# Kernel optimization log

Hardware: AMD Instinct MI355X
Metric: run time of the kernel (lower is better)

The kernel has to match this reference:

```python
import jax, jax.numpy as jnp
import numpy as np

B, V, C, H, W, D = 2, 3, 8, 128, 160, 64


def bilinear_sample(feat, grid):
    """feat: [B,C,H,W]; grid: [B,N,2] normalized to [-1,1], align_corners=True,
    padding_mode='zeros' (matches F.grid_sample). Returns [B,C,N]."""
    b, c, h, w = feat.shape
    ix = (grid[..., 0] + 1.0) * 0.5 * (w - 1)  # [B,N]
    iy = (grid[..., 1] + 1.0) * 0.5 * (h - 1)
    x0 = jnp.floor(ix)
    y0 = jnp.floor(iy)
    wx1 = ix - x0
    wy1 = iy - y0
    flat = feat.reshape(b, c, h * w)

    def corner(xi, yi, wgt):
        valid = (xi >= 0) & (xi <= w - 1) & (yi >= 0) & (yi <= h - 1)
        xc = jnp.clip(xi, 0, w - 1).astype(jnp.int32)
        yc = jnp.clip(yi, 0, h - 1).astype(jnp.int32)
        idx = yc * w + xc  # [B,N]
        vals = jnp.take_along_axis(flat, jnp.broadcast_to(idx[:, None, :], (b, c, idx.shape[1])), axis=2)
        return vals * (wgt * valid.astype(feat.dtype))[:, None, :]

    out = (corner(x0, y0, (1 - wx1) * (1 - wy1))
           + corner(x0 + 1, y0, wx1 * (1 - wy1))
           + corner(x0, y0 + 1, (1 - wx1) * wy1)
           + corner(x0 + 1, y0 + 1, wx1 * wy1))
    return out


def homo_warping(src_feat, proj_mat, depth_values):
    """src_feat [B,C,H,W], proj_mat [B,3,4], depth_values [B,D,H,W].
    Returns warped volume [B,C,D,H,W] and normalized grid [B,D,H,W,2]."""
    b, c, h, w = src_feat.shape
    d = depth_values.shape[1]
    R = proj_mat[:, :, :3]
    T = proj_mat[:, :, 3:]  # [B,3,1]
    ys, xs = jnp.meshgrid(jnp.arange(h, dtype=src_feat.dtype),
                          jnp.arange(w, dtype=src_feat.dtype), indexing='ij')
    ref = jnp.stack([xs.ravel(), ys.ravel(), jnp.ones(h * w, src_feat.dtype)], 0)  # [3,HW]
    Rp = jnp.einsum('bij,jp->bip', R, ref)  # [B,3,HW]
    dv = depth_values.reshape(b, d, h * w)
    src = Rp[:, :, None, :] + T[:, :, :, None] / dv[:, None, :, :]  # [B,3,D,HW]
    xy = src[:, :2] / src[:, 2:3]
    gx = xy[:, 0] / ((w - 1) / 2.0) - 1.0
    gy = xy[:, 1] / ((h - 1) / 2.0) - 1.0
    grid = jnp.stack([gx, gy], axis=-1)  # [B,D,HW,2]
    warped = bilinear_sample(src_feat, grid.reshape(b, d * h * w, 2)).reshape(b, c, d, h, w)
    return warped, grid.reshape(b, d, h, w, 2)


def setup_inputs() -> dict:
    key = jax.random.key(0)
    k1, k2, k3, k4, k5 = jax.random.split(key, 5)
    features = jax.random.normal(k1, (V, B, C, H, W), dtype=jnp.float32)
    # near-identity projective maps so warps land mostly in-bounds
    eye = jnp.broadcast_to(jnp.eye(3, dtype=jnp.float32), (B, V, 3, 3))
    Rm = eye + 0.01 * jax.random.normal(k2, (B, V, 3, 3), dtype=jnp.float32)
    Tm = 2.0 * jax.random.normal(k3, (B, V, 3, 1), dtype=jnp.float32)
    proj_matrices = jnp.concatenate([Rm, Tm], axis=-1)  # [B,V,3,4]
    base = jnp.linspace(2.0, 10.0, D, dtype=jnp.float32)[None, :, None, None]
    depth_values = base + 0.1 * jax.random.uniform(k4, (B, D, H, W), dtype=jnp.float32)
    reg_weight = jax.random.normal(k5, (C,), dtype=jnp.float32)
    return {"features": features, "proj_matrices": proj_matrices,
            "depth_values": depth_values, "reg_weight": reg_weight,
            "num_depth": D}


def reference(features, proj_matrices, depth_values, reg_weight, num_depth):
    v = features.shape[0]
    ref_feat = features[0]
    b, c, h, w = ref_feat.shape
    d = num_depth
    ref_volume = jnp.broadcast_to(ref_feat[:, :, None], (b, c, d, h, w))
    volume_sum = ref_volume
    volume_sq_sum = ref_volume ** 2
    in_masks = jnp.ones((b, 1, d, h, w), dtype=ref_feat.dtype)
    for i in range(1, v):  # fixed small number of source views
        warped, grid = homo_warping(features[i], proj_matrices[:, i], depth_values)
        m = (grid > -1.0) & (grid < 1.0)
        in_masks = in_masks + (m[..., 0] & m[..., 1]).astype(ref_feat.dtype)[:, None]
        volume_sum = volume_sum + warped
        volume_sq_sum = volume_sq_sum + warped ** 2
    count = 1.0 / in_masks
    volume_feat = volume_sq_sum * count - (volume_sum * count) ** 2  # [B,C,D,H,W]
    # stand-in cost regularization: channel reduction -> [B,D,H,W]
    cost = jnp.einsum('bcdhw,c->bdhw', volume_feat, reg_weight)
    prob_volume = jax.nn.softmax(cost, axis=1)
    depth = jnp.sum(prob_volume * depth_values, axis=1)  # [B,H,W]
    return depth
```

## Files before the change

kernel.cpp:

```cpp
#include <hip/hip_runtime.h>
#include <math.h>

#define BB 2
#define VV 3
#define CC 8
#define HH 128
#define WW 160
#define DD 64
constexpr int HW = HH * WW;
constexpr int NPIX = BB * HW;
constexpr int PIXBANDS = NPIX / 256;
constexpr int BANDS_PER_XCD = PIXBANDS / 8;

typedef _Float16 h8 __attribute__((ext_vector_type(8)));

static __device__ __forceinline__ h8 splat8(float x) {
    const _Float16 v = (_Float16)x;
    h8 r = {v, v, v, v, v, v, v, v};
    return r;
}

__global__ __launch_bounds__(256)
void transpose_feats(const float* __restrict__ feats, h8* __restrict__ ft)
{
    const int t = blockIdx.x * blockDim.x + threadIdx.x;
    if (t >= VV * BB * HW) return;
    const int vb = t / HW;
    const int hw = t - vb * HW;
    const float* src = feats + (size_t)vb * CC * HW + hw;
    h8 v;
#pragma unroll
    for (int c = 0; c < CC; ++c) v[c] = (_Float16)src[(size_t)c * HW];
    ft[(size_t)vb * HW + hw] = v;
}

__global__ __launch_bounds__(256)
void cost_kernel(const h8* __restrict__ ft,
                 const float* __restrict__ proj,
                 const float* __restrict__ depthv,
                 const float* __restrict__ regw,
                 float* __restrict__ cost_out)
{
    const int i    = blockIdx.x;
    const int xcd  = i & 7;
    const int idx  = i >> 3;
    const int band = xcd * BANDS_PER_XCD + (idx % BANDS_PER_XCD);
    const int d    = idx / BANDS_PER_XCD;
    const int pixel = band * 256 + threadIdx.x;

    const int b  = (pixel >= HW) ? 1 : 0;
    const int hw = pixel - b * HW;
    const int h  = hw / WW;
    const int w  = hw - h * WW;

    float rf[CC], rf2[CC];
    {
        h8 rv = ft[(size_t)b * HW + hw];
#pragma unroll
        for (int c = 0; c < CC; ++c) { rf[c] = (float)rv[c]; rf2[c] = rf[c] * rf[c]; }
    }

    float Rp[2][3], Tv[2][3];
    const float xf = (float)w, yf = (float)h;
#pragma unroll
    for (int v = 0; v < 2; ++v) {
        const float* M = proj + ((size_t)b * VV + (v + 1)) * 12;
#pragma unroll
        for (int j = 0; j < 3; ++j) {
            Rp[v][j] = M[j * 4 + 0] * xf + M[j * 4 + 1] * yf + M[j * 4 + 2];
            Tv[v][j] = M[j * 4 + 3];
        }
    }

    const h8* fsrc0 = ft + (size_t)(1 * BB + b) * HW;
    const h8* fsrc1 = ft + (size_t)(2 * BB + b) * HW;

    const float dv = depthv[(size_t)b * DD * HW + (size_t)d * HW + hw];
    const float inv_dv = __builtin_amdgcn_rcpf(dv);

    float wt[2][4];
    int   ib[2][4];
    float nmask = 1.0f;
#pragma unroll
    for (int v = 0; v < 2; ++v) {
        const float sx = Rp[v][0] + Tv[v][0] * inv_dv;
        const float sy = Rp[v][1] + Tv[v][1] * inv_dv;
        const float sz = Rp[v][2] + Tv[v][2] * inv_dv;
        const float rsz = __builtin_amdgcn_rcpf(sz);
        const float ix = sx * rsz;
        const float iy = sy * rsz;
        nmask += ((ix > 0.f) && (ix < (float)(WW - 1)) &&
                  (iy > 0.f) && (iy < (float)(HH - 1))) ? 1.0f : 0.0f;
        const float x0f = floorf(ix), y0f = floorf(iy);
        const float wx1 = ix - x0f, wy1 = iy - y0f;
        const float wx0 = 1.f - wx1, wy0 = 1.f - wy1;
        const float x1f = x0f + 1.f, y1f = y0f + 1.f;
        const bool vx0 = (x0f >= 0.f) && (x0f <= (float)(WW - 1));
        const bool vx1 = (x1f >= 0.f) && (x1f <= (float)(WW - 1));
        const bool vy0 = (y0f >= 0.f) && (y0f <= (float)(HH - 1));
        const bool vy1 = (y1f >= 0.f) && (y1f <= (float)(HH - 1));
        wt[v][0] = wx0 * wy0 * ((vx0 && vy0) ? 1.f : 0.f);
        wt[v][1] = wx1 * wy0 * ((vx1 && vy0) ? 1.f : 0.f);
        wt[v][2] = wx0 * wy1 * ((vx0 && vy1) ? 1.f : 0.f);
        wt[v][3] = wx1 * wy1 * ((vx1 && vy1) ? 1.f : 0.f);
        const int x0c = (int)fminf(fmaxf(x0f, 0.f), (float)(WW - 1));
        const int x1c = (int)fminf(fmaxf(x1f, 0.f), (float)(WW - 1));
        const int y0c = (int)fminf(fmaxf(y0f, 0.f), (float)(HH - 1));
        const int y1c = (int)fminf(fmaxf(y1f, 0.f), (float)(HH - 1));
        ib[v][0] = y0c * WW + x0c;
        ib[v][1] = y0c * WW + x1c;
        ib[v][2] = y1c * WW + x0c;
        ib[v][3] = y1c * WW + x1c;
    }

    h8 a0 = fsrc0[ib[0][0]];
    h8 a1 = fsrc0[ib[0][1]];
    h8 a2 = fsrc0[ib[0][2]];
    h8 a3 = fsrc0[ib[0][3]];
    h8 b0 = fsrc1[ib[1][0]];
    h8 b1 = fsrc1[ib[1][1]];
    h8 b2 = fsrc1[ib[1][2]];
    h8 b3 = fsrc1[ib[1][3]];

    h8 vah = a0 * splat8(wt[0][0]) + a1 * splat8(wt[0][1])
           + a2 * splat8(wt[0][2]) + a3 * splat8(wt[0][3]);
    h8 vbh = b0 * splat8(wt[1][0]) + b1 * splat8(wt[1][1])
           + b2 * splat8(wt[1][2]) + b3 * splat8(wt[1][3]);

    const float cnt = __builtin_amdgcn_rcpf(nmask);
    float t1 = 0.f, t2 = 0.f;
#pragma unroll
    for (int c = 0; c < CC; ++c) {
        const float av = (float)vah[c];
        const float bv = (float)vbh[c];
        const float sum = rf[c] + av + bv;
        const float sq  = rf2[c] + av * av + bv * bv;
        t1 += regw[c] * sq;
        t2 += (regw[c] * sum) * sum;
    }
    const float cost = cnt * t1 - (cnt * cnt) * t2;

    cost_out[(size_t)b * DD * HW + (size_t)d * HW + hw] = cost;
}

__global__ __launch_bounds__(256)
void softmax_depth(const float* __restrict__ cost,
                   const float* __restrict__ depthv,
                   float* __restrict__ out)
{
    const int t     = blockIdx.x * blockDim.x + threadIdx.x;
    const int lane  = t & 63;
    const int waveg = t >> 6;
    const int px    = lane & 15;
    const int chunk = lane >> 4;
    const int pixel = waveg * 16 + px;

    const int b  = (pixel >= HW) ? 1 : 0;
    const int hw = pixel - b * HW;

    const float* cp = cost   + (size_t)b * DD * HW + hw;
    const float* dp = depthv + (size_t)b * DD * HW + hw;

    float m = -INFINITY, l = 0.f, s = 0.f;
#pragma unroll 4
    for (int j = 0; j < 16; ++j) {
        const int d = chunk * 16 + j;
        const float c  = cp[(size_t)d * HW];
        const float dv = dp[(size_t)d * HW];
        const float M = fmaxf(m, c);
        const float e_old = __expf(m - M);
        const float e_new = __expf(c - M);
        l = l * e_old + e_new;
        s = s * e_old + e_new * dv;
        m = M;
    }

#pragma unroll
    for (int off = 16; off < 64; off <<= 1) {
        const float m2 = __shfl_xor(m, off, 64);
        const float l2 = __shfl_xor(l, off, 64);
        const float s2 = __shfl_xor(s, off, 64);
        const float M  = fmaxf(m, m2);
        const float e1 = __expf(m - M);
        const float e2 = __expf(m2 - M);
        l = l * e1 + l2 * e2;
        s = s * e1 + s2 * e2;
        m = M;
    }

    if (chunk == 0) out[pixel] = s / l;
}

extern "C" void kernel_launch(void* const* d_in, const int* in_sizes, int n_in,
                              void* d_out, int out_size, void* d_ws, size_t ws_size,
                              hipStream_t stream) {
    const float* feats  = (const float*)d_in[0];
    const float* proj   = (const float*)d_in[1];
    const float* depthv = (const float*)d_in[2];
    const float* regw   = (const float*)d_in[3];
    float* out = (float*)d_out;
    h8*    ft   = (h8*)d_ws;
    float* cost = (float*)((char*)d_ws + (size_t)VV * BB * HW * sizeof(h8));

    {
        const int n = VV * BB * HW;
        hipLaunchKernelGGL(transpose_feats, dim3((n + 255) / 256), dim3(256), 0, stream,
                           feats, ft);
    }
    {
        const int grid = DD * PIXBANDS;
        hipLaunchKernelGGL(cost_kernel, dim3(grid), dim3(256), 0, stream,
                           ft, proj, depthv, regw, cost);
    }
    {
        const int total = NPIX * 4;
        hipLaunchKernelGGL(softmax_depth, dim3(total / 256), dim3(256), 0, stream,
                           cost, depthv, out);
    }
}
```

Baseline: 103.0 us.

## Process two depths per thread, reuse gathers, pack fp16 cost with depth

Each cost-kernel thread now handles two consecutive depth planes. It reuses the eight source-view gathers when the second depth lands on the same bilinear cell, and halves the grid size. The cost and depth value are written together as a packed fp16 pair, so the softmax kernel reads one 4-byte stream instead of two fp32 streams. This cuts gather traffic and intermediate bandwidth, at the cost of fp16 rounding of cost and depth before the softmax, more register pressure, and divergent reload branches.

```diff
diff --git a/kernel.cpp b/kernel.cpp
--- a/kernel.cpp
+++ b/kernel.cpp
@@ -13,6 +13,7 @@
 constexpr int BANDS_PER_XCD = PIXBANDS / 8;
 
 typedef _Float16 h8 __attribute__((ext_vector_type(8)));
+typedef _Float16 h2 __attribute__((ext_vector_type(2)));
 
 static __device__ __forceinline__ h8 splat8(float x) {
     const _Float16 v = (_Float16)x;
@@ -39,13 +40,14 @@
                  const float* __restrict__ proj,
                  const float* __restrict__ depthv,
                  const float* __restrict__ regw,
-                 float* __restrict__ cost_out)
+                 h2* __restrict__ pc)
 {
     const int i    = blockIdx.x;
     const int xcd  = i & 7;
     const int idx  = i >> 3;
     const int band = xcd * BANDS_PER_XCD + (idx % BANDS_PER_XCD);
-    const int d    = idx / BANDS_PER_XCD;
+    const int dp   = idx / BANDS_PER_XCD;
+    const int d0   = dp * 2;
     const int pixel = band * 256 + threadIdx.x;
 
     const int b  = (pixel >= HW) ? 1 : 0;
@@ -60,92 +62,138 @@
         for (int c = 0; c < CC; ++c) { rf[c] = (float)rv[c]; rf2[c] = rf[c] * rf[c]; }
     }
 
-    float Rp[2][3], Tv[2][3];
+    float Rp[2][3], Tvv[2][3];
     const float xf = (float)w, yf = (float)h;
 #pragma unroll
     for (int v = 0; v < 2; ++v) {
         const float* M = proj + ((size_t)b * VV + (v + 1)) * 12;
 #pragma unroll
         for (int j = 0; j < 3; ++j) {
-            Rp[v][j] = M[j * 4 + 0] * xf + M[j * 4 + 1] * yf + M[j * 4 + 2];
-            Tv[v][j] = M[j * 4 + 3];
+            Rp[v][j]  = M[j * 4 + 0] * xf + M[j * 4 + 1] * yf + M[j * 4 + 2];
+            Tvv[v][j] = M[j * 4 + 3];
         }
     }
 
     const h8* fsrc0 = ft + (size_t)(1 * BB + b) * HW;
     const h8* fsrc1 = ft + (size_t)(2 * BB + b) * HW;
 
-    const float dv = depthv[(size_t)b * DD * HW + (size_t)d * HW + hw];
-    const float inv_dv = __builtin_amdgcn_rcpf(dv);
-
-    float wt[2][4];
-    int   ib[2][4];
-    float nmask = 1.0f;
+    const size_t dvbase = (size_t)b * DD * HW + hw;
+    const float dvA = depthv[dvbase + (size_t)d0 * HW];
+    const float dvB = depthv[dvbase + (size_t)(d0 + 1) * HW];
+    const float invA = __builtin_amdgcn_rcpf(dvA);
+    const float invB = __builtin_amdgcn_rcpf(dvB);
+
+    float wtA[2][4], wtB[2][4];
+    int   ibA[2][4], ibB[2][4];
+    float nmA = 1.0f, nmB = 1.0f;
 #pragma unroll
     for (int v = 0; v < 2; ++v) {
-        const float sx = Rp[v][0] + Tv[v][0] * inv_dv;
-        const float sy = Rp[v][1] + Tv[v][1] * inv_dv;
-        const float sz = Rp[v][2] + Tv[v][2] * inv_dv;
-        const float rsz = __builtin_amdgcn_rcpf(sz);
-        const float ix = sx * rsz;
-        const float iy = sy * rsz;
-        nmask += ((ix > 0.f) && (ix < (float)(WW - 1)) &&
-                  (iy > 0.f) && (iy < (float)(HH - 1))) ? 1.0f : 0.0f;
-        const float x0f = floorf(ix), y0f = floorf(iy);
-        const float wx1 = ix - x0f, wy1 = iy - y0f;
-        const float wx0 = 1.f - wx1, wy0 = 1.f - wy1;
-        const float x1f = x0f + 1.f, y1f = y0f + 1.f;
-        const bool vx0 = (x0f >= 0.f) && (x0f <= (float)(WW - 1));
-        const bool vx1 = (x1f >= 0.f) && (x1f <= (float)(WW - 1));
-        const bool vy0 = (y0f >= 0.f) && (y0f <= (float)(HH - 1));
-        const bool vy1 = (y1f >= 0.f) && (y1f <= (float)(HH - 1));
-        wt[v][0] = wx0 * wy0 * ((vx0 && vy0) ? 1.f : 0.f);
-        wt[v][1] = wx1 * wy0 * ((vx1 && vy0) ? 1.f : 0.f);
-        wt[v][2] = wx0 * wy1 * ((vx0 && vy1) ? 1.f : 0.f);
-        wt[v][3] = wx1 * wy1 * ((vx1 && vy1) ? 1.f : 0.f);
-        const int x0c = (int)fminf(fmaxf(x0f, 0.f), (float)(WW - 1));
-        const int x1c = (int)fminf(fmaxf(x1f, 0.f), (float)(WW - 1));
-        const int y0c = (int)fminf(fmaxf(y0f, 0.f), (float)(HH - 1));
-        const int y1c = (int)fminf(fmaxf(y1f, 0.f), (float)(HH - 1));
-        ib[v][0] = y0c * WW + x0c;
-        ib[v][1] = y0c * WW + x1c;
-        ib[v][2] = y1c * WW + x0c;
-        ib[v][3] = y1c * WW + x1c;
-    }
-
-    h8 a0 = fsrc0[ib[0][0]];
-    h8 a1 = fsrc0[ib[0][1]];
-    h8 a2 = fsrc0[ib[0][2]];
-    h8 a3 = fsrc0[ib[0][3]];
-    h8 b0 = fsrc1[ib[1][0]];
-    h8 b1 = fsrc1[ib[1][1]];
-    h8 b2 = fsrc1[ib[1][2]];
-    h8 b3 = fsrc1[ib[1][3]];
-
-    h8 vah = a0 * splat8(wt[0][0]) + a1 * splat8(wt[0][1])
-           + a2 * splat8(wt[0][2]) + a3 * splat8(wt[0][3]);
-    h8 vbh = b0 * splat8(wt[1][0]) + b1 * splat8(wt[1][1])
-           + b2 * splat8(wt[1][2]) + b3 * splat8(wt[1][3]);
-
-    const float cnt = __builtin_amdgcn_rcpf(nmask);
-    float t1 = 0.f, t2 = 0.f;
-#pragma unroll
-    for (int c = 0; c < CC; ++c) {
-        const float av = (float)vah[c];
-        const float bv = (float)vbh[c];
-        const float sum = rf[c] + av + bv;
-        const float sq  = rf2[c] + av * av + bv * bv;
-        t1 += regw[c] * sq;
-        t2 += (regw[c] * sum) * sum;
-    }
-    const float cost = cnt * t1 - (cnt * cnt) * t2;
-
-    cost_out[(size_t)b * DD * HW + (size_t)d * HW + hw] = cost;
+#pragma unroll
+        for (int pass = 0; pass < 2; ++pass) {
+            const float inv_dv = pass ? invB : invA;
+            float (&wt)[2][4] = pass ? wtB : wtA;
+            int   (&ib)[2][4] = pass ? ibB : ibA;
+            float &nm = pass ? nmB : nmA;
+            const float sx = Rp[v][0] + Tvv[v][0] * inv_dv;
+            const float sy = Rp[v][1] + Tvv[v][1] * inv_dv;
+            const float sz = Rp[v][2] + Tvv[v][2] * inv_dv;
+            const float rsz = __builtin_amdgcn_rcpf(sz);
+            const float ix = sx * rsz;
+            const float iy = sy * rsz;
+            nm += ((ix > 0.f) && (ix < (float)(WW - 1)) &&
+                   (iy > 0.f) && (iy < (float)(HH - 1))) ? 1.0f : 0.0f;
+            const float x0f = floorf(ix), y0f = floorf(iy);
+            const float wx1 = ix - x0f, wy1 = iy - y0f;
+            const float wx0 = 1.f - wx1, wy0 = 1.f - wy1;
+            const float x1f = x0f + 1.f, y1f = y0f + 1.f;
+            const bool vx0 = (x0f >= 0.f) && (x0f <= (float)(WW - 1));
+            const bool vx1 = (x1f >= 0.f) && (x1f <= (float)(WW - 1));
+            const bool vy0 = (y0f >= 0.f) && (y0f <= (float)(HH - 1));
+            const bool vy1 = (y1f >= 0.f) && (y1f <= (float)(HH - 1));
+            wt[v][0] = wx0 * wy0 * ((vx0 && vy0) ? 1.f : 0.f);
+            wt[v][1] = wx1 * wy0 * ((vx1 && vy0) ? 1.f : 0.f);
+            wt[v][2] = wx0 * wy1 * ((vx0 && vy1) ? 1.f : 0.f);
+            wt[v][3] = wx1 * wy1 * ((vx1 && vy1) ? 1.f : 0.f);
+            const int x0c = (int)fminf(fmaxf(x0f, 0.f), (float)(WW - 1));
+            const int x1c = (int)fminf(fmaxf(x1f, 0.f), (float)(WW - 1));
+            const int y0c = (int)fminf(fmaxf(y0f, 0.f), (float)(HH - 1));
+            const int y1c = (int)fminf(fmaxf(y1f, 0.f), (float)(HH - 1));
+            ib[v][0] = y0c * WW + x0c;
+            ib[v][1] = y0c * WW + x1c;
+            ib[v][2] = y1c * WW + x0c;
+            ib[v][3] = y1c * WW + x1c;
+        }
+    }
+
+    h8 a0 = fsrc0[ibA[0][0]];
+    h8 a1 = fsrc0[ibA[0][1]];
+    h8 a2 = fsrc0[ibA[0][2]];
+    h8 a3 = fsrc0[ibA[0][3]];
+    h8 b0 = fsrc1[ibA[1][0]];
+    h8 b1 = fsrc1[ibA[1][1]];
+    h8 b2 = fsrc1[ibA[1][2]];
+    h8 b3 = fsrc1[ibA[1][3]];
+
+    const size_t obase = (size_t)b * DD * HW + hw;
+
+    {
+        h8 vah = a0 * splat8(wtA[0][0]) + a1 * splat8(wtA[0][1])
+               + a2 * splat8(wtA[0][2]) + a3 * splat8(wtA[0][3]);
+        h8 vbh = b0 * splat8(wtA[1][0]) + b1 * splat8(wtA[1][1])
+               + b2 * splat8(wtA[1][2]) + b3 * splat8(wtA[1][3]);
+        const float cnt = __builtin_amdgcn_rcpf(nmA);
+        float t1 = 0.f, t2 = 0.f;
+#pragma unroll
+        for (int c = 0; c < CC; ++c) {
+            const float av = (float)vah[c];
+            const float bv = (float)vbh[c];
+            const float sum = rf[c] + av + bv;
+            const float sq  = rf2[c] + av * av + bv * bv;
+            t1 += regw[c] * sq;
+            t2 += (regw[c] * sum) * sum;
+        }
+        const float cost = cnt * t1 - (cnt * cnt) * t2;
+        h2 pck; pck[0] = (_Float16)cost; pck[1] = (_Float16)dvA;
+        pc[obase + (size_t)d0 * HW] = pck;
+    }
+
+    if (ibB[0][0] != ibA[0][0] || ibB[0][3] != ibA[0][3]) {
+        a0 = fsrc0[ibB[0][0]];
+        a1 = fsrc0[ibB[0][1]];
+        a2 = fsrc0[ibB[0][2]];
+        a3 = fsrc0[ibB[0][3]];
+    }
+    if (ibB[1][0] != ibA[1][0] || ibB[1][3] != ibA[1][3]) {
+        b0 = fsrc1[ibB[1][0]];
+        b1 = fsrc1[ibB[1][1]];
+        b2 = fsrc1[ibB[1][2]];
+        b3 = fsrc1[ibB[1][3]];
+    }
+
+    {
+        h8 vah = a0 * splat8(wtB[0][0]) + a1 * splat8(wtB[0][1])
+               + a2 * splat8(wtB[0][2]) + a3 * splat8(wtB[0][3]);
+        h8 vbh = b0 * splat8(wtB[1][0]) + b1 * splat8(wtB[1][1])
+               + b2 * splat8(wtB[1][2]) + b3 * splat8(wtB[1][3]);
+        const float cnt = __builtin_amdgcn_rcpf(nmB);
+        float t1 = 0.f, t2 = 0.f;
+#pragma unroll
+        for (int c = 0; c < CC; ++c) {
+            const float av = (float)vah[c];
+            const float bv = (float)vbh[c];
+            const float sum = rf[c] + av + bv;
+            const float sq  = rf2[c] + av * av + bv * bv;
+            t1 += regw[c] * sq;
+            t2 += (regw[c] * sum) * sum;
+        }
+        const float cost = cnt * t1 - (cnt * cnt) * t2;
+        h2 pck; pck[0] = (_Float16)cost; pck[1] = (_Float16)dvB;
+        pc[obase + (size_t)(d0 + 1) * HW] = pck;
+    }
 }
 
 __global__ __launch_bounds__(256)
-void softmax_depth(const float* __restrict__ cost,
-                   const float* __restrict__ depthv,
+void softmax_depth(const h2* __restrict__ pc,
                    float* __restrict__ out)
 {
     const int t     = blockIdx.x * blockDim.x + threadIdx.x;
@@ -158,15 +206,15 @@
     const int b  = (pixel >= HW) ? 1 : 0;
     const int hw = pixel - b * HW;
 
-    const float* cp = cost   + (size_t)b * DD * HW + hw;
-    const float* dp = depthv + (size_t)b * DD * HW + hw;
+    const h2* cp = pc + (size_t)b * DD * HW + hw;
 
     float m = -INFINITY, l = 0.f, s = 0.f;
 #pragma unroll 4
     for (int j = 0; j < 16; ++j) {
         const int d = chunk * 16 + j;
-        const float c  = cp[(size_t)d * HW];
-        const float dv = dp[(size_t)d * HW];
+        const h2 v = cp[(size_t)d * HW];
+        const float c  = (float)v[0];
+        const float dv = (float)v[1];
         const float M = fmaxf(m, c);
         const float e_old = __expf(m - M);
         const float e_new = __expf(c - M);
@@ -199,8 +247,8 @@
     const float* depthv = (const float*)d_in[2];
     const float* regw   = (const float*)d_in[3];
     float* out = (float*)d_out;
-    h8*    ft   = (h8*)d_ws;
-    float* cost = (float*)((char*)d_ws + (size_t)VV * BB * HW * sizeof(h8));
+    h8* ft = (h8*)d_ws;
+    h2* pc = (h2*)((char*)d_ws + (size_t)VV * BB * HW * sizeof(h8));
 
     {
         const int n = VV * BB * HW;
@@ -208,13 +256,13 @@
                            feats, ft);
     }
     {
-        const int grid = DD * PIXBANDS;
+        const int grid = (DD / 2) * PIXBANDS;
         hipLaunchKernelGGL(cost_kernel, dim3(grid), dim3(256), 0, stream,
-                           ft, proj, depthv, regw, cost);
+                           ft, proj, depthv, regw, pc);
     }
     {
         const int total = NPIX * 4;
         hipLaunchKernelGGL(softmax_depth, dim3(total / 256), dim3(256), 0, stream,
-                           cost, depthv, out);
-    }
-}
+                           pc, out);
+    }
+}
```

Result: faster. 96.70 us (-6.1%).

## Process four depths per thread, reuse gathers, pack fp16 cost and depth

Applied to the files above, without the earlier changes.

Each cost-kernel thread now handles four consecutive depth planes. It skips reloading the bilinear corner features when the sampled indices match the previous depth. The projection is rewritten to multiply by depth instead of dividing by it, which drops one reciprocal per depth. Cost and depth are written together as one packed fp16 pair, so the softmax kernel reads half the intermediate bytes and no longer rereads the fp32 depth tensor. The trade-off is fp16 precision for cost and depth values, plus fewer blocks in the cost kernel.

```diff
diff --git a/kernel.cpp b/kernel.cpp
--- a/kernel.cpp
+++ b/kernel.cpp
@@ -11,8 +11,10 @@
 constexpr int NPIX = BB * HW;
 constexpr int PIXBANDS = NPIX / 256;
 constexpr int BANDS_PER_XCD = PIXBANDS / 8;
+constexpr int DPT = 4;
 
 typedef _Float16 h8 __attribute__((ext_vector_type(8)));
+typedef _Float16 h2 __attribute__((ext_vector_type(2)));
 
 static __device__ __forceinline__ h8 splat8(float x) {
     const _Float16 v = (_Float16)x;
@@ -39,13 +41,14 @@
                  const float* __restrict__ proj,
                  const float* __restrict__ depthv,
                  const float* __restrict__ regw,
-                 float* __restrict__ cost_out)
+                 h2* __restrict__ pc)
 {
     const int i    = blockIdx.x;
     const int xcd  = i & 7;
     const int idx  = i >> 3;
     const int band = xcd * BANDS_PER_XCD + (idx % BANDS_PER_XCD);
-    const int d    = idx / BANDS_PER_XCD;
+    const int dq   = idx / BANDS_PER_XCD;
+    const int d0   = dq * DPT;
     const int pixel = band * 256 + threadIdx.x;
 
     const int b  = (pixel >= HW) ? 1 : 0;
@@ -60,92 +63,106 @@
         for (int c = 0; c < CC; ++c) { rf[c] = (float)rv[c]; rf2[c] = rf[c] * rf[c]; }
     }
 
-    float Rp[2][3], Tv[2][3];
+    float Rp[2][3], Tvv[2][3];
     const float xf = (float)w, yf = (float)h;
 #pragma unroll
     for (int v = 0; v < 2; ++v) {
         const float* M = proj + ((size_t)b * VV + (v + 1)) * 12;
 #pragma unroll
         for (int j = 0; j < 3; ++j) {
-            Rp[v][j] = M[j * 4 + 0] * xf + M[j * 4 + 1] * yf + M[j * 4 + 2];
-            Tv[v][j] = M[j * 4 + 3];
+            Rp[v][j]  = M[j * 4 + 0] * xf + M[j * 4 + 1] * yf + M[j * 4 + 2];
+            Tvv[v][j] = M[j * 4 + 3];
         }
     }
 
     const h8* fsrc0 = ft + (size_t)(1 * BB + b) * HW;
     const h8* fsrc1 = ft + (size_t)(2 * BB + b) * HW;
 
-    const float dv = depthv[(size_t)b * DD * HW + (size_t)d * HW + hw];
-    const float inv_dv = __builtin_amdgcn_rcpf(dv);
-
-    float wt[2][4];
-    int   ib[2][4];
-    float nmask = 1.0f;
-#pragma unroll
-    for (int v = 0; v < 2; ++v) {
-        const float sx = Rp[v][0] + Tv[v][0] * inv_dv;
-        const float sy = Rp[v][1] + Tv[v][1] * inv_dv;
-        const float sz = Rp[v][2] + Tv[v][2] * inv_dv;
-        const float rsz = __builtin_amdgcn_rcpf(sz);
-        const float ix = sx * rsz;
-        const float iy = sy * rsz;
-        nmask += ((ix > 0.f) && (ix < (float)(WW - 1)) &&
-                  (iy > 0.f) && (iy < (float)(HH - 1))) ? 1.0f : 0.0f;
-        const float x0f = floorf(ix), y0f = floorf(iy);
-        const float wx1 = ix - x0f, wy1 = iy - y0f;
-        const float wx0 = 1.f - wx1, wy0 = 1.f - wy1;
-        const float x1f = x0f + 1.f, y1f = y0f + 1.f;
-        const bool vx0 = (x0f >= 0.f) && (x0f <= (float)(WW - 1));
-        const bool vx1 = (x1f >= 0.f) && (x1f <= (float)(WW - 1));
-        const bool vy0 = (y0f >= 0.f) && (y0f <= (float)(HH - 1));
-        const bool vy1 = (y1f >= 0.f) && (y1f <= (float)(HH - 1));
-        wt[v][0] = wx0 * wy0 * ((vx0 && vy0) ? 1.f : 0.f);
-        wt[v][1] = wx1 * wy0 * ((vx1 && vy0) ? 1.f : 0.f);
-        wt[v][2] = wx0 * wy1 * ((vx0 && vy1) ? 1.f : 0.f);
-        wt[v][3] = wx1 * wy1 * ((vx1 && vy1) ? 1.f : 0.f);
-        const int x0c = (int)fminf(fmaxf(x0f, 0.f), (float)(WW - 1));
-        const int x1c = (int)fminf(fmaxf(x1f, 0.f), (float)(WW - 1));
-        const int y0c = (int)fminf(fmaxf(y0f, 0.f), (float)(HH - 1));
-        const int y1c = (int)fminf(fmaxf(y1f, 0.f), (float)(HH - 1));
-        ib[v][0] = y0c * WW + x0c;
-        ib[v][1] = y0c * WW + x1c;
-        ib[v][2] = y1c * WW + x0c;
-        ib[v][3] = y1c * WW + x1c;
-    }
-
-    h8 a0 = fsrc0[ib[0][0]];
-    h8 a1 = fsrc0[ib[0][1]];
-    h8 a2 = fsrc0[ib[0][2]];
-    h8 a3 = fsrc0[ib[0][3]];
-    h8 b0 = fsrc1[ib[1][0]];
-    h8 b1 = fsrc1[ib[1][1]];
-    h8 b2 = fsrc1[ib[1][2]];
-    h8 b3 = fsrc1[ib[1][3]];
-
-    h8 vah = a0 * splat8(wt[0][0]) + a1 * splat8(wt[0][1])
-           + a2 * splat8(wt[0][2]) + a3 * splat8(wt[0][3]);
-    h8 vbh = b0 * splat8(wt[1][0]) + b1 * splat8(wt[1][1])
-           + b2 * splat8(wt[1][2]) + b3 * splat8(wt[1][3]);
-
-    const float cnt = __builtin_amdgcn_rcpf(nmask);
-    float t1 = 0.f, t2 = 0.f;
-#pragma unroll
-    for (int c = 0; c < CC; ++c) {
-        const float av = (float)vah[c];
-        const float bv = (float)vbh[c];
-        const float sum = rf[c] + av + bv;
-        const float sq  = rf2[c] + av * av + bv * bv;
-        t1 += regw[c] * sq;
-        t2 += (regw[c] * sum) * sum;
-    }
-    const float cost = cnt * t1 - (cnt * cnt) * t2;
-
-    cost_out[(size_t)b * DD * HW + (size_t)d * HW + hw] = cost;
+    const float* dvp = depthv + (size_t)b * DD * HW + hw;
+    float dvv[DPT];
+#pragma unroll
+    for (int k = 0; k < DPT; ++k) dvv[k] = dvp[(size_t)(d0 + k) * HW];
+
+    const size_t obase = (size_t)b * DD * HW + hw;
+
+    h8 A0, A1, A2, A3, B0, B1, B2, B3;
+    int pa0 = -1, pa3 = -1, pb0 = -1, pb3 = -1;
+
+#pragma unroll
+    for (int k = 0; k < DPT; ++k) {
+        const float d = dvv[k];
+
+        float wt[2][4];
+        int   ib[2][4];
+        float nmask = 1.0f;
+#pragma unroll
+        for (int v = 0; v < 2; ++v) {
+            const float sx = Rp[v][0] * d + Tvv[v][0];
+            const float sy = Rp[v][1] * d + Tvv[v][1];
+            const float sz = Rp[v][2] * d + Tvv[v][2];
+            const float rsz = __builtin_amdgcn_rcpf(sz);
+            const float ix = sx * rsz;
+            const float iy = sy * rsz;
+            nmask += ((ix > 0.f) && (ix < (float)(WW - 1)) &&
+                      (iy > 0.f) && (iy < (float)(HH - 1))) ? 1.0f : 0.0f;
+            const float x0f = floorf(ix), y0f = floorf(iy);
+            const float wx1 = ix - x0f, wy1 = iy - y0f;
+            const float wx0 = 1.f - wx1, wy0 = 1.f - wy1;
+            const float x1f = x0f + 1.f, y1f = y0f + 1.f;
+            const bool vx0 = (x0f >= 0.f) && (x0f <= (float)(WW - 1));
+            const bool vx1 = (x1f >= 0.f) && (x1f <= (float)(WW - 1));
+            const bool vy0 = (y0f >= 0.f) && (y0f <= (float)(HH - 1));
+            const bool vy1 = (y1f >= 0.f) && (y1f <= (float)(HH - 1));
+            wt[v][0] = wx0 * wy0 * ((vx0 && vy0) ? 1.f : 0.f);
+            wt[v][1] = wx1 * wy0 * ((vx1 && vy0) ? 1.f : 0.f);
+            wt[v][2] = wx0 * wy1 * ((vx0 && vy1) ? 1.f : 0.f);
+            wt[v][3] = wx1 * wy1 * ((vx1 && vy1) ? 1.f : 0.f);
+            const int x0c = (int)fminf(fmaxf(x0f, 0.f), (float)(WW - 1));
+            const int x1c = (int)fminf(fmaxf(x1f, 0.f), (float)(WW - 1));
+            const int y0c = (int)fminf(fmaxf(y0f, 0.f), (float)(HH - 1));
+            const int y1c = (int)fminf(fmaxf(y1f, 0.f), (float)(HH - 1));
+            ib[v][0] = y0c * WW + x0c;
+            ib[v][1] = y0c * WW + x1c;
+            ib[v][2] = y1c * WW + x0c;
+            ib[v][3] = y1c * WW + x1c;
+        }
+
+        if (ib[0][0] != pa0 || ib[0][3] != pa3) {
+            A0 = fsrc0[ib[0][0]]; A1 = fsrc0[ib[0][1]];
+            A2 = fsrc0[ib[0][2]]; A3 = fsrc0[ib[0][3]];
+            pa0 = ib[0][0]; pa3 = ib[0][3];
+        }
+        if (ib[1][0] != pb0 || ib[1][3] != pb3) {
+            B0 = fsrc1[ib[1][0]]; B1 = fsrc1[ib[1][1]];
+            B2 = fsrc1[ib[1][2]]; B3 = fsrc1[ib[1][3]];
+            pb0 = ib[1][0]; pb3 = ib[1][3];
+        }
+
+        h8 vah = A0 * splat8(wt[0][0]) + A1 * splat8(wt[0][1])
+               + A2 * splat8(wt[0][2]) + A3 * splat8(wt[0][3]);
+        h8 vbh = B0 * splat8(wt[1][0]) + B1 * splat8(wt[1][1])
+               + B2 * splat8(wt[1][2]) + B3 * splat8(wt[1][3]);
+
+        const float cnt = __builtin_amdgcn_rcpf(nmask);
+        float t1 = 0.f, t2 = 0.f;
+#pragma unroll
+        for (int c = 0; c < CC; ++c) {
+            const float av = (float)vah[c];
+            const float bv = (float)vbh[c];
+            const float sum = rf[c] + av + bv;
+            const float sq  = rf2[c] + av * av + bv * bv;
+            t1 += regw[c] * sq;
+            t2 += (regw[c] * sum) * sum;
+        }
+        const float cost = cnt * t1 - (cnt * cnt) * t2;
+
+        h2 pck; pck[0] = (_Float16)cost; pck[1] = (_Float16)d;
+        pc[obase + (size_t)(d0 + k) * HW] = pck;
+    }
 }
 
 __global__ __launch_bounds__(256)
-void softmax_depth(const float* __restrict__ cost,
-                   const float* __restrict__ depthv,
+void softmax_depth(const h2* __restrict__ pc,
                    float* __restrict__ out)
 {
     const int t     = blockIdx.x * blockDim.x + threadIdx.x;
@@ -158,15 +175,15 @@
     const int b  = (pixel >= HW) ? 1 : 0;
     const int hw = pixel - b * HW;
 
-    const float* cp = cost   + (size_t)b * DD * HW + hw;
-    const float* dp = depthv + (size_t)b * DD * HW + hw;
+    const h2* cp = pc + (size_t)b * DD * HW + hw;
 
     float m = -INFINITY, l = 0.f, s = 0.f;
 #pragma unroll 4
     for (int j = 0; j < 16; ++j) {
         const int d = chunk * 16 + j;
-        const float c  = cp[(size_t)d * HW];
-        const float dv = dp[(size_t)d * HW];
+        const h2 v = cp[(size_t)d * HW];
+        const float c  = (float)v[0];
+        const float dv = (float)v[1];
         const float M = fmaxf(m, c);
         const float e_old = __expf(m - M);
         const float e_new = __expf(c - M);
@@ -199,8 +216,8 @@
     const float* depthv = (const float*)d_in[2];
     const float* regw   = (const float*)d_in[3];
     float* out = (float*)d_out;
-    h8*    ft   = (h8*)d_ws;
-    float* cost = (float*)((char*)d_ws + (size_t)VV * BB * HW * sizeof(h8));
+    h8* ft = (h8*)d_ws;
+    h2* pc = (h2*)((char*)d_ws + (size_t)VV * BB * HW * sizeof(h8));
 
     {
         const int n = VV * BB * HW;
@@ -208,13 +225,13 @@
                            feats, ft);
     }
     {
-        const int grid = DD * PIXBANDS;
+        const int grid = (DD / DPT) * PIXBANDS;
         hipLaunchKernelGGL(cost_kernel, dim3(grid), dim3(256), 0, stream,
-                           ft, proj, depthv, regw, cost);
+                           ft, proj, depthv, regw, pc);
     }
     {
         const int total = NPIX * 4;
         hipLaunchKernelGGL(softmax_depth, dim3(total / 256), dim3(256), 0, stream,
-                           cost, depthv, out);
-    }
-}
+                           pc, out);
+    }
+}
```

After: 96.42 us. -6.4%, faster.
